# Kernel tuning notes

Hardware: AMD Instinct MI355X
Metric: run time of the kernel (lower is better)

## Reference

```python
import jax, jax.numpy as jnp
import numpy as np

T, K, D, CIN = 8, 64, 512, 1536  # timesteps, num_centers, redu_dim, input channels


def _conv(x, w, b=None, pad=0):
    y = jax.lax.conv_general_dilated(x, w, (1, 1), [(pad, pad), (pad, pad)],
                                     dimension_numbers=('NCHW', 'OIHW', 'NCHW'))
    return y if b is None else y + b[None, :, None, None]


def setup_inputs() -> dict:
    key = jax.random.key(0)
    ks = jax.random.split(key, 15)
    B, H, W = 32, 8, 8
    s = lambda i, shp: jax.random.normal(ks[i], shp, jnp.float32) * 0.05
    return dict(
        x=jax.random.normal(ks[0], (B * T, CIN, H, W), jnp.float32),
        redu_w=s(1, (D, CIN, 1, 1)), redu_b=s(2, (D,)),
        w_x=s(3, (K, D, 1, 1)),
        att_x=s(4, (K, K, 3, 3)), att_h_w=s(5, (K, K, 3, 3)), att_b=s(6, (K,)),
        share_w=s(7, (K, K, 3, 3)), share_b=s(8, (K,)),
        U_r=s(9, (K, K, 3, 3)), U_z=s(10, (K, K, 3, 3)), U_h=s(11, (K, K, 3, 3)),
        centers=s(12, (K, D)),
        fc1_w=s(13, (T * K // 16, T * K)), fc2_w=s(14, (T * K, T * K // 16)),
    )


def reference(x, redu_w, redu_b, w_x, att_x, att_h_w, att_b, share_w, share_b,
              U_r, U_z, U_h, centers, fc1_w, fc2_w):
    NT, _, H, W = x.shape
    B = NT // T
    xt = _conv(x, redu_w, redu_b)                    # (B*T, D, H, W) 1x1 reduction
    wxpb = _conv(xt, w_x)                            # (B*T, K, H, W)
    att_v = _conv(wxpb, att_x, pad=1).reshape(B, T, K, H, W).transpose(1, 0, 2, 3, 4)  # (T,B,K,H,W)
    wxpb5 = wxpb.reshape(B, T, K, H, W)

    def fc(v):  # ChannelAttention shared MLP (1x1 convs == matmuls)
        return jnp.maximum(v @ fc1_w.T, 0.) @ fc2_w.T

    def step(h, _):
        ah = _conv(h, att_h_w, att_b, pad=1)               # (B,K,H,W)
        e = jax.nn.relu(att_v + ah[None])                  # (T,B,K,H,W)
        e = e.transpose(1, 0, 2, 3, 4).reshape(B, T * K, H * W)
        g = jnp.tanh(fc(e.mean(-1)) + fc(e.max(-1)))       # (B, T*K) channel attention
        ex = jnp.exp(g.reshape(B, T, K))
        den = ex.sum(1, keepdims=True)
        den = den + (den == 0).astype(ex.dtype)
        alphas = ex / den                                  # softmax over timesteps
        wxt = (alphas[:, :, :, None, None] * wxpb5).sum(1) # (B,K,H,W)
        wxt = _conv(wxt, share_w, share_b, pad=1)
        z = jax.nn.sigmoid(wxt + _conv(h, U_z, pad=1))
        r = jax.nn.sigmoid(wxt + _conv(h, U_r, pad=1))
        hh = jnp.tanh(wxt + _conv(r * h, U_h, pad=1))
        h_new = (1. - z) * hh + z * h
        return h_new, h_new

    h0 = jnp.zeros((B, K, H, W), x.dtype)
    _, hs = jax.lax.scan(step, h0, None, length=T)         # (T,B,K,H,W)
    assigns = hs.transpose(1, 0, 2, 3, 4).reshape(B * T, K, H * W)
    a_sum = assigns.sum(-1, keepdims=True)                 # (B*T,K,1)
    a = a_sum * centers[None]                              # (B*T,K,D)
    feats = xt.reshape(B * T, D, H * W).transpose(0, 2, 1) # (B*T,HW,D)
    vlad = jnp.einsum('nks,nsd->nkd', assigns, feats) - a  # (B*T,K,D)
    vlad = vlad.reshape(B, T, K, D).sum(1)                 # (B,K,D)
    vlad = vlad / jnp.maximum(jnp.linalg.norm(vlad, axis=2, keepdims=True), 1e-12)
    vlad = vlad.reshape(B, K * D)
    vlad = vlad / jnp.maximum(jnp.linalg.norm(vlad, axis=1, keepdims=True), 1e-12)
    return vlad
```

## Files before the change

kernel.cpp:

```cpp
#include <hip/hip_runtime.h>
#include <math.h>

#define T_   8
#define K_   64
#define D_   512
#define CIN_ 1536
#define B_   32
#define S_   64
#define NT_  256

#define WLO_BF16  786432u
#define WXT_OFF   786432u
#define XT_OFF    819200u
#define WXPB_OFF  9207808u
#define ATTV_OFF  10256384u
#define HS_OFF    11436032u
#define ASUM_OFF  13041664u
#define WPB       25034752u

typedef __bf16 v8bf __attribute__((ext_vector_type(8)));
typedef __bf16 v4bf __attribute__((ext_vector_type(4)));
typedef float  v4f  __attribute__((ext_vector_type(4)));
typedef _Float16 v4h __attribute__((ext_vector_type(4)));
typedef _Float16 v8h __attribute__((ext_vector_type(8)));

__global__ __launch_bounds__(256) void k_prep(const float* __restrict__ redu_w,
                                              const float* __restrict__ w_x,
                                              float* __restrict__ ws) {
    unsigned idx = blockIdx.x * 256u + threadIdx.x;
    if (idx < 786432u) {
        float f = redu_w[idx];
        __bf16 h = (__bf16)f;
        __bf16 l = (__bf16)(f - (float)h);
        __bf16* wb = (__bf16*)ws;
        wb[idx] = h;
        wb[WLO_BF16 + idx] = l;
    } else if (idx < 819200u) {
        unsigned i = idx - 786432u;
        unsigned dd = i >> 6, k = i & 63u;
        ws[WXT_OFF + i] = w_x[k * 512u + dd];
    }
}

__global__ __launch_bounds__(256) void k_prep_w(const float* __restrict__ w0,
                                                const float* __restrict__ w1,
                                                const float* __restrict__ w2,
                                                const float* __restrict__ w3,
                                                const float* __restrict__ w4,
                                                float* __restrict__ ws) {
    unsigned idx = blockIdx.x * 256u + threadIdx.x;
    if (idx >= 184320u) return;
    unsigned w = idx / 36864u, r = idx % 36864u;
    const float* src = (w == 0) ? w0 : (w == 1) ? w1 : (w == 2) ? w2 : (w == 3) ? w3 : w4;
    float f = src[r];
    __bf16 h = (__bf16)f;
    __bf16 l = (__bf16)(f - (float)h);
    unsigned o = r / 576u, rem = r % 576u, ii = rem / 9u, dydx = rem % 9u;
    __bf16* wb = (__bf16*)ws;
    unsigned dst = WPB + w * 73728u + (dydx * 64u + o) * 64u + ii;
    wb[dst] = h;
    wb[dst + 36864u] = l;
}

__global__ __launch_bounds__(256) void k_gemm_xt_mfma(const float* __restrict__ x,
                                                      const float* __restrict__ redu_b,
                                                      float* __restrict__ ws) {
    __shared__ __bf16 xhi_s[64 * 72];
    __shared__ __bf16 xlo_s[64 * 72];
    const __bf16* __restrict__ Whi = (const __bf16*)ws;
    const __bf16* __restrict__ Wlo = ((const __bf16*)ws) + WLO_BF16;
    float* xt = ws + XT_OFF;
    const int n = blockIdx.y;
    const int d0 = blockIdx.x * 256;
    const int tid = threadIdx.x;
    const int wave = tid >> 6, lane = tid & 63;
    const int lrow = lane & 15, lkg = lane >> 4;
    const int m_base = d0 + wave * 64;
    const float* __restrict__ xn = x + n * 98304;
    const int s4 = tid & 15, cb = tid >> 4;

    v4f acc[4][4];
#pragma unroll
    for (int mt = 0; mt < 4; ++mt)
#pragma unroll
        for (int nt = 0; nt < 4; ++nt) acc[mt][nt] = (v4f){0.f, 0.f, 0.f, 0.f};

    for (int c0 = 0; c0 < 1536; c0 += 64) {
        float4 v[4];
#pragma unroll
        for (int j = 0; j < 4; ++j)
            v[j] = *(const float4*)&xn[(c0 + cb * 4 + j) * 64 + s4 * 4];
        __syncthreads();
#pragma unroll
        for (int i = 0; i < 4; ++i) {
            v4bf hv, lv;
#pragma unroll
            for (int j = 0; j < 4; ++j) {
                float f = ((const float*)&v[j])[i];
                __bf16 h = (__bf16)f;
                hv[j] = h;
                lv[j] = (__bf16)(f - (float)h);
            }
            int row = s4 * 4 + i;
            *(v4bf*)&xhi_s[row * 72 + cb * 4] = hv;
            *(v4bf*)&xlo_s[row * 72 + cb * 4] = lv;
        }
        __syncthreads();
#pragma unroll
        for (int ks = 0; ks < 64; ks += 32) {
            v8bf bh[4], bl[4], ah[4], al[4];
#pragma unroll
            for (int nt = 0; nt < 4; ++nt) {
                int off = (nt * 16 + lrow) * 72 + ks + lkg * 8;
                bh[nt] = *(const v8bf*)&xhi_s[off];
                bl[nt] = *(const v8bf*)&xlo_s[off];
            }
#pragma unroll
            for (int mt = 0; mt < 4; ++mt) {
                int gi = (m_base + mt * 16 + lrow) * 1536 + c0 + ks + lkg * 8;
                ah[mt] = *(const v8bf*)&Whi[gi];
                al[mt] = *(const v8bf*)&Wlo[gi];
            }
#pragma unroll
            for (int mt = 0; mt < 4; ++mt)
#pragma unroll
                for (int nt = 0; nt < 4; ++nt) {
                    acc[mt][nt] = __builtin_amdgcn_mfma_f32_16x16x32_bf16(
                        ah[mt], bh[nt], acc[mt][nt], 0, 0, 0);
                    acc[mt][nt] = __builtin_amdgcn_mfma_f32_16x16x32_bf16(
                        ah[mt], bl[nt], acc[mt][nt], 0, 0, 0);
                    acc[mt][nt] = __builtin_amdgcn_mfma_f32_16x16x32_bf16(
                        al[mt], bh[nt], acc[mt][nt], 0, 0, 0);
                }
        }
    }
#pragma unroll
    for (int mt = 0; mt < 4; ++mt) {
#pragma unroll
        for (int r = 0; r < 4; ++r) {
            int m = m_base + mt * 16 + lkg * 4 + r;
            float bias = redu_b[m];
#pragma unroll
            for (int nt = 0; nt < 4; ++nt) {
                int s = nt * 16 + lrow;
                xt[(n * 512 + m) * 64 + s] = acc[mt][nt][r] + bias;
            }
        }
    }
}

__global__ __launch_bounds__(256) void k_gemm_wxpb(float* __restrict__ ws) {
    __shared__ float Aw[16 * 64];
    __shared__ float Bx[16 * 64];
    const float* wxT = ws + WXT_OFF;
    const float* xt = ws + XT_OFF;
    float* wxpb = ws + WXPB_OFF;
    const int n = blockIdx.x;
    const int tid = threadIdx.x;
    const int sg = tid & 15, kg = tid >> 4;

    float acc[4][4];
#pragma unroll
    for (int i = 0; i < 4; ++i)
#pragma unroll
        for (int j = 0; j < 4; ++j) acc[i][j] = 0.f;

    for (int d0 = 0; d0 < 512; d0 += 16) {
        int cc = tid >> 4, q = tid & 15;
        *(float4*)&Aw[cc * 64 + q * 4] = *(const float4*)&wxT[(d0 + cc) * 64 + q * 4];
        *(float4*)&Bx[cc * 64 + q * 4] = *(const float4*)&xt[n * 32768 + (d0 + cc) * 64 + q * 4];
        __syncthreads();
#pragma unroll
        for (int c2 = 0; c2 < 16; ++c2) {
            float4 a = *(const float4*)&Aw[c2 * 64 + kg * 4];
            float4 b = *(const float4*)&Bx[c2 * 64 + sg * 4];
            float av[4] = {a.x, a.y, a.z, a.w};
            float bv[4] = {b.x, b.y, b.z, b.w};
#pragma unroll
            for (int i = 0; i < 4; ++i)
#pragma unroll
                for (int j = 0; j < 4; ++j)
                    acc[i][j] = fmaf(av[i], bv[j], acc[i][j]);
        }
        __syncthreads();
    }
#pragma unroll
    for (int i = 0; i < 4; ++i) {
        float4 o = {acc[i][0], acc[i][1], acc[i][2], acc[i][3]};
        *(float4*)&wxpb[(n * 64 + kg * 4 + i) * 64 + sg * 4] = o;
    }
}

__global__ __launch_bounds__(128) void k_conv3x3(const float* __restrict__ in,
                                                 const float* __restrict__ wt,
                                                 const float* __restrict__ bias,
                                                 float* __restrict__ out) {
    __shared__ float in_s[4096];
    __shared__ float w_s[16 * 576];
    const int img = blockIdx.y;
    const int k0 = blockIdx.x * 16;
    const int tid = threadIdx.x;
    const int kl = tid >> 3, y = tid & 7;
#pragma unroll
    for (int i = 0; i < 8; ++i) {
        int f = tid + i * 128;
        *(float4*)&in_s[f * 4] = *(const float4*)&in[img * 4096 + f * 4];
    }
#pragma unroll
    for (int i = 0; i < 18; ++i) {
        int f = tid + i * 128;
        *(float4*)&w_s[f * 4] = *(const float4*)&wt[k0 * 576 + f * 4];
    }
    __syncthreads();
    float o[8];
#pragma unroll
    for (int xx = 0; xx < 8; ++xx) o[xx] = 0.f;
    for (int kp = 0; kp < 64; ++kp) {
        const float* wp = &w_s[kl * 576 + kp * 9];
        float wv[9];
#pragma unroll
        for (int q = 0; q < 9; ++q) wv[q] = wp[q];
#pragma unroll
        for (int dy = 0; dy < 3; ++dy) {
            int yy = y + dy - 1;
            if (yy >= 0 && yy < 8) {
                float4 ra = *(const float4*)&in_s[kp * 64 + yy * 8];
                float4 rb = *(const float4*)&in_s[kp * 64 + yy * 8 + 4];
                float r[8] = {ra.x, ra.y, ra.z, ra.w, rb.x, rb.y, rb.z, rb.w};
                float wa = wv[dy * 3 + 0], wb = wv[dy * 3 + 1], wc = wv[dy * 3 + 2];
#pragma unroll
                for (int xx = 0; xx < 8; ++xx) {
                    float t = wb * r[xx];
                    if (xx > 0) t += wa * r[xx - 1];
                    if (xx < 7) t += wc * r[xx + 1];
                    o[xx] += t;
                }
            }
        }
    }
    float bv = bias ? bias[k0 + kl] : 0.f;
    float4 o0 = {o[0] + bv, o[1] + bv, o[2] + bv, o[3] + bv};
    float4 o1 = {o[4] + bv, o[5] + bv, o[6] + bv, o[7] + bv};
    *(float4*)&out[img * 4096 + (k0 + kl) * 64 + y * 8] = o0;
    *(float4*)&out[img * 4096 + (k0 + kl) * 64 + y * 8 + 4] = o1;
}

__device__ __forceinline__ void conv_mfma(const __bf16* __restrict__ Wh,
                                          const __bf16* tS,
                                          int l15, int kg8, int mt, v4f acc[4]) {
    v8bf vz;
#pragma unroll
    for (int q = 0; q < 8; ++q) vz[q] = (__bf16)0.f;
#pragma unroll
    for (int i = 0; i < 4; ++i) acc[i] = (v4f){0.f, 0.f, 0.f, 0.f};
    const int yb = l15 >> 3, xb = l15 & 7;
    v8bf wh[9][2];
#pragma unroll
    for (int p = 0; p < 9; ++p) {
        const int wrow = (p * 64 + mt * 16 + l15) * 64 + kg8;
#pragma unroll
        for (int kci = 0; kci < 2; ++kci)
            wh[p][kci] = *(const v8bf*)&Wh[wrow + kci * 32];
    }
#pragma unroll
    for (int dy = 0; dy < 3; ++dy)
#pragma unroll
        for (int dx = 0; dx < 3; ++dx) {
            const int x0 = xb + dx - 1;
            const bool okx = (unsigned)x0 < 8u;
#pragma unroll
            for (int i = 0; i < 4; ++i) {
                const int y0 = yb + dy - 1 + 2 * i;
                const bool ok = ((unsigned)y0 < 8u) & okx;
                const int s0 = ((y0 * 8 + x0) & 63) * 72 + kg8;
#pragma unroll
                for (int kci = 0; kci < 2; ++kci) {
                    v8bf b = ok ? *(const v8bf*)&tS[s0 + kci * 32] : vz;
                    acc[i] = __builtin_amdgcn_mfma_f32_16x16x32_bf16(
                        wh[dy * 3 + dx][kci], b, acc[i], 0, 0, 0);
                }
            }
        }
}

__device__ __forceinline__ void conv_mfma3(const __bf16* __restrict__ W0,
                                           const __bf16* __restrict__ W1,
                                           const __bf16* __restrict__ W2,
                                           const __bf16* tS,
                                           int l15, int kg8, int mt,
                                           v4f a0[4], v4f a1[4], v4f a2[4]) {
    v8bf vz;
#pragma unroll
    for (int q = 0; q < 8; ++q) vz[q] = (__bf16)0.f;
#pragma unroll
    for (int i = 0; i < 4; ++i) {
        a0[i] = (v4f){0.f, 0.f, 0.f, 0.f};
        a1[i] = (v4f){0.f, 0.f, 0.f, 0.f};
        a2[i] = (v4f){0.f, 0.f, 0.f, 0.f};
    }
    const int yb = l15 >> 3, xb = l15 & 7;
#pragma unroll
    for (int dy = 0; dy < 3; ++dy) {
        v8bf w0[3][2], w1[3][2], w2[3][2];
#pragma unroll
        for (int dx = 0; dx < 3; ++dx) {
            const int wrow = ((dy * 3 + dx) * 64 + mt * 16 + l15) * 64 + kg8;
#pragma unroll
            for (int kci = 0; kci < 2; ++kci) {
                w0[dx][kci] = *(const v8bf*)&W0[wrow + kci * 32];
                w1[dx][kci] = *(const v8bf*)&W1[wrow + kci * 32];
                w2[dx][kci] = *(const v8bf*)&W2[wrow + kci * 32];
            }
        }
#pragma unroll
        for (int dx = 0; dx < 3; ++dx) {
            const int x0 = xb + dx - 1;
            const bool okx = (unsigned)x0 < 8u;
#pragma unroll
            for (int i = 0; i < 4; ++i) {
                const int y0 = yb + dy - 1 + 2 * i;
                const bool ok = ((unsigned)y0 < 8u) & okx;
                const int s0 = ((y0 * 8 + x0) & 63) * 72 + kg8;
#pragma unroll
                for (int kci = 0; kci < 2; ++kci) {
                    v8bf b = ok ? *(const v8bf*)&tS[s0 + kci * 32] : vz;
                    a0[i] = __builtin_amdgcn_mfma_f32_16x16x32_bf16(w0[dx][kci], b, a0[i], 0, 0, 0);
                    a1[i] = __builtin_amdgcn_mfma_f32_16x16x32_bf16(w1[dx][kci], b, a1[i], 0, 0, 0);
                    a2[i] = __builtin_amdgcn_mfma_f32_16x16x32_bf16(w2[dx][kci], b, a2[i], 0, 0, 0);
                }
            }
        }
    }
}

__global__ __launch_bounds__(256) void k_recur(const float* __restrict__ att_b,
                                               const float* __restrict__ share_b,
                                               const float* __restrict__ fc1_w,
                                               const float* __restrict__ fc2_w,
                                               float* __restrict__ ws) {
    __shared__ float h_s[4096];
    __shared__ __attribute__((aligned(16))) __bf16 tA[64 * 72];
    __shared__ float cA[64 * 65];
    __shared__ float cB[64 * 65];
    __shared__ float misc[1088];
    __shared__ __attribute__((aligned(16))) _Float16 attv_s[32768];
    const int b = blockIdx.x, tid = threadIdx.x;
    const int lane = tid & 63;
    const int wave = tid >> 6;
    const int mt = wave;
    const int l15 = lane & 15, kg = lane >> 4, kg8 = kg * 8;
    const __bf16* Wp = (const __bf16*)ws + WPB;
    const float* attv = ws + ATTV_OFF;
    const float* wxpb = ws + WXPB_OFF;
    float* hsg = ws + HS_OFF;
    float* asg = ws + ASUM_OFF;

    {
        const float* src = attv + b * 32768;
        for (int i = tid; i < 8192; i += 256) {
            float4 v = *(const float4*)&src[i * 4];
            v4h h4 = {(_Float16)v.x, (_Float16)v.y, (_Float16)v.z, (_Float16)v.w};
            *(v4h*)&attv_s[i * 4] = h4;
        }
    }

    for (int i = tid; i < 4096; i += 256) h_s[i] = 0.f;
    float abvr[2];
#pragma unroll
    for (int rep = 0; rep < 2; ++rep) abvr[rep] = att_b[(tid + rep * 256) >> 3];
    float sb4[4];
#pragma unroll
    for (int r = 0; r < 4; ++r) sb4[r] = share_b[mt * 16 + kg * 4 + r];
    __syncthreads();

    for (int t = 0; t < 8; ++t) {
#pragma unroll
        for (int rep = 0; rep < 2; ++rep) {
            int s = tid & 63, g = (tid >> 6) + rep * 4;
#pragma unroll
            for (int q4 = 0; q4 < 2; ++q4) {
                v4bf hv;
#pragma unroll
                for (int q = 0; q < 4; ++q) hv[q] = (__bf16)h_s[(g * 8 + q4 * 4 + q) * 64 + s];
                *(v4bf*)&tA[s * 72 + g * 8 + q4 * 4] = hv;
            }
        }
        __syncthreads();
        v4f az[4], ar[4];
        {
            v4f a[4];
            conv_mfma3(Wp, Wp + 2u * 73728u, Wp + 3u * 73728u, tA,
                       l15, kg8, mt, a, az, ar);
#pragma unroll
            for (int i = 0; i < 4; ++i)
#pragma unroll
                for (int r = 0; r < 4; ++r)
                    cA[(mt * 16 + kg * 4 + r) * 65 + i * 16 + l15] = a[i][r];
        }
        __syncthreads();
#pragma unroll
        for (int rep = 0; rep < 2; ++rep) {
            int vt = tid + rep * 256;
            int kk = vt >> 3, yy = vt & 7;
            float ah8[8];
            const float* cr = &cA[kk * 65 + yy * 8];
#pragma unroll
            for (int xx = 0; xx < 8; ++xx) ah8[xx] = cr[xx] + abvr[rep];
            for (int tp = 0; tp < 8; ++tp) {
                v8h va = *(const v8h*)&attv_s[tp * 4096 + kk * 64 + yy * 8];
                float s_ = 0.f, m_ = 0.f;
#pragma unroll
                for (int xx = 0; xx < 8; ++xx) {
                    float v = fmaxf((float)va[xx] + ah8[xx], 0.f);
                    s_ += v;
                    m_ = fmaxf(m_, v);
                }
                s_ += __shfl_down(s_, 4, 8);
                s_ += __shfl_down(s_, 2, 8);
                s_ += __shfl_down(s_, 1, 8);
                m_ = fmaxf(m_, __shfl_down(m_, 4, 8));
                m_ = fmaxf(m_, __shfl_down(m_, 2, 8));
                m_ = fmaxf(m_, __shfl_down(m_, 1, 8));
                if (yy == 0) {
                    misc[tp * 64 + kk] = s_ * (1.f / 64.f);
                    misc[512 + tp * 64 + kk] = m_;
                }
            }
        }
        __syncthreads();
        {
            int i2 = tid >> 2, part = tid & 3;
            int i = i2 & 31;
            const float* src = misc + ((i2 < 32) ? 0 : 512);
            const float* wrow = fc1_w + i * 512 + part * 128;
            const float* s2 = src + part * 128;
            float p = 0.f;
#pragma unroll
            for (int c4 = 0; c4 < 32; ++c4) {
                float4 wv = *(const float4*)&wrow[c4 * 4];
                float4 sv = *(const float4*)&s2[c4 * 4];
                p = fmaf(wv.x, sv.x, p);
                p = fmaf(wv.y, sv.y, p);
                p = fmaf(wv.z, sv.z, p);
                p = fmaf(wv.w, sv.w, p);
            }
            p += __shfl_down(p, 2, 4);
            p += __shfl_down(p, 1, 4);
            if (part == 0) misc[1024 + i2] = fmaxf(p, 0.f);
        }
        __syncthreads();
#pragma unroll
        for (int rep = 0; rep < 2; ++rep) {
            int vt = tid + rep * 256;
            const float* w2 = fc2_w + vt * 32;
            float gm = 0.f, gx = 0.f;
#pragma unroll
            for (int i4 = 0; i4 < 8; ++i4) {
                float4 wv = *(const float4*)&w2[i4 * 4];
                gm = fmaf(wv.x, misc[1024 + i4 * 4 + 0], gm);
                gm = fmaf(wv.y, misc[1024 + i4 * 4 + 1], gm);
                gm = fmaf(wv.z, misc[1024 + i4 * 4 + 2], gm);
                gm = fmaf(wv.w, misc[1024 + i4 * 4 + 3], gm);
                gx = fmaf(wv.x, misc[1056 + i4 * 4 + 0], gx);
                gx = fmaf(wv.y, misc[1056 + i4 * 4 + 1], gx);
                gx = fmaf(wv.z, misc[1056 + i4 * 4 + 2], gx);
                gx = fmaf(wv.w, misc[1056 + i4 * 4 + 3], gx);
            }
            misc[vt] = expf(tanhf(gm + gx));
        }
        __syncthreads();
#pragma unroll
        for (int rep = 0; rep < 2; ++rep) {
            int vt = tid + rep * 256;
            int k6 = vt & 63;
            float den = 0.f;
#pragma unroll
            for (int tp = 0; tp < 8; ++tp) den += misc[tp * 64 + k6];
            den += (den == 0.f) ? 1.f : 0.f;
            misc[512 + vt] = misc[vt] / den;
        }
        __syncthreads();
#pragma unroll
        for (int rep = 0; rep < 2; ++rep) {
            int vt = tid + rep * 256;
            int kk = vt >> 3, yy = vt & 7;
            float wx8[8];
#pragma unroll
            for (int xx = 0; xx < 8; ++xx) wx8[xx] = 0.f;
            const float* src0 = wxpb + b * 32768 + kk * 64 + yy * 8;
#pragma unroll
            for (int tp = 0; tp < 8; ++tp) {
                float al = misc[512 + tp * 64 + kk];
                float4 v0 = *(const float4*)&src0[tp * 4096];
                float4 v1 = *(const float4*)&src0[tp * 4096 + 4];
                float v[8] = {v0.x, v0.y, v0.z, v0.w, v1.x, v1.y, v1.z, v1.w};
#pragma unroll
                for (int xx = 0; xx < 8; ++xx) wx8[xx] = fmaf(al, v[xx], wx8[xx]);
            }
#pragma unroll
            for (int xx = 0; xx < 8; ++xx) tA[(yy * 8 + xx) * 72 + kk] = (__bf16)wx8[xx];
        }
        __syncthreads();
        v4f ash[4];
        conv_mfma(Wp + 1u * 73728u, tA, l15, kg8, mt, ash);
        float zf[4][4], wof[4][4];
#pragma unroll
        for (int i = 0; i < 4; ++i)
#pragma unroll
            for (int r = 0; r < 4; ++r) {
                int ko = mt * 16 + kg * 4 + r;
                int s = i * 16 + l15;
                float wo = ash[i][r] + sb4[r];
                float z = 1.f / (1.f + expf(-(wo + az[i][r])));
                float rr = 1.f / (1.f + expf(-(wo + ar[i][r])));
                cB[ko * 65 + s] = rr * h_s[ko * 64 + s];
                zf[i][r] = z;
                wof[i][r] = wo;
            }
        __syncthreads();
#pragma unroll
        for (int rep = 0; rep < 2; ++rep) {
            int s = tid & 63, g = (tid >> 6) + rep * 4;
#pragma unroll
            for (int q4 = 0; q4 < 2; ++q4) {
                v4bf hv;
#pragma unroll
                for (int q = 0; q < 4; ++q) hv[q] = (__bf16)cB[(g * 8 + q4 * 4 + q) * 65 + s];
                *(v4bf*)&tA[s * 72 + g * 8 + q4 * 4] = hv;
            }
        }
        __syncthreads();
        {
            v4f ach[4];
            conv_mfma(Wp + 4u * 73728u, tA, l15, kg8, mt, ach);
#pragma unroll
            for (int r = 0; r < 4; ++r) {
                int ko = mt * 16 + kg * 4 + r;
                float rsum = 0.f;
#pragma unroll
                for (int i = 0; i < 4; ++i) {
                    int s = i * 16 + l15;
                    float hh = tanhf(wof[i][r] + ach[i][r]);
                    float hold = h_s[ko * 64 + s];
                    float hn = (1.f - zf[i][r]) * hh + zf[i][r] * hold;
                    h_s[ko * 64 + s] = hn;
                    hsg[((t * 32 + b) * 64 + ko) * 64 + s] = hn;
                    rsum += hn;
                }
                rsum += __shfl_xor(rsum, 8, 16);
                rsum += __shfl_xor(rsum, 4, 16);
                rsum += __shfl_xor(rsum, 2, 16);
                rsum += __shfl_xor(rsum, 1, 16);
                if (l15 == 0) misc[1024 + ko] = rsum;
            }
        }
        __syncthreads();
        if (tid < 64) asg[b * 512 + t * 64 + tid] = misc[1024 + tid];
        __syncthreads();
    }
}

__global__ __launch_bounds__(256) void k_vlad(const float* __restrict__ centers,
                                              const float* __restrict__ ws,
                                              float* __restrict__ out) {
    __shared__ float As[16 * 68];
    __shared__ float Bs[16 * 68];
    const int b = blockIdx.y;
    const int d0 = blockIdx.x * 64;
    const int tid = threadIdx.x;
    const int kq = tid & 15, dq = tid >> 4;
    const int lk = tid >> 2, q = tid & 3;
    const float* hs = ws + HS_OFF;
    const float* xt = ws + XT_OFF;
    float acc[4][4];
#pragma unroll
    for (int i = 0; i < 4; ++i)
#pragma unroll
        for (int j = 0; j < 4; ++j) acc[i][j] = 0.f;

    for (int rc = 0; rc < 512; rc += 16) {
        int t = rc >> 6, hw0 = rc & 63;
        float4 va = *(const float4*)&hs[((t * 32 + b) * 64 + lk) * 64 + hw0 + q * 4];
        float4 vb = *(const float4*)&xt[(b * 8 + t) * 32768 + (d0 + lk) * 64 + hw0 + q * 4];
        __syncthreads();
        As[(q * 4 + 0) * 68 + lk] = va.x;
        As[(q * 4 + 1) * 68 + lk] = va.y;
        As[(q * 4 + 2) * 68 + lk] = va.z;
        As[(q * 4 + 3) * 68 + lk] = va.w;
        Bs[(q * 4 + 0) * 68 + lk] = vb.x;
        Bs[(q * 4 + 1) * 68 + lk] = vb.y;
        Bs[(q * 4 + 2) * 68 + lk] = vb.z;
        Bs[(q * 4 + 3) * 68 + lk] = vb.w;
        __syncthreads();
#pragma unroll
        for (int cc = 0; cc < 16; ++cc) {
            float4 a = *(const float4*)&As[cc * 68 + kq * 4];
            float4 bb = *(const float4*)&Bs[cc * 68 + dq * 4];
            float av[4] = {a.x, a.y, a.z, a.w};
            float bv[4] = {bb.x, bb.y, bb.z, bb.w};
#pragma unroll
            for (int i = 0; i < 4; ++i)
#pragma unroll
                for (int j = 0; j < 4; ++j)
                    acc[i][j] = fmaf(av[i], bv[j], acc[i][j]);
        }
    }
    const float* asum = ws + ASUM_OFF;
#pragma unroll
    for (int i = 0; i < 4; ++i) {
        int k = kq * 4 + i;
        float at = 0.f;
#pragma unroll
        for (int tp = 0; tp < 8; ++tp) at += asum[b * 512 + tp * 64 + k];
        float4 cen = *(const float4*)&centers[k * 512 + d0 + dq * 4];
        float4 o = {acc[i][0] - at * cen.x, acc[i][1] - at * cen.y,
                    acc[i][2] - at * cen.z, acc[i][3] - at * cen.w};
        *(float4*)&out[b * 32768 + k * 512 + d0 + dq * 4] = o;
    }
}

__global__ __launch_bounds__(64) void k_norm1(float* __restrict__ out) {
    const int b = blockIdx.x >> 6, k = blockIdx.x & 63;
    float* p = out + b * 32768 + k * 512;
    const int tid = threadIdx.x;
    float v[8];
    float ss = 0.f;
#pragma unroll
    for (int i = 0; i < 8; ++i) {
        v[i] = p[tid + i * 64];
        ss = fmaf(v[i], v[i], ss);
    }
#pragma unroll
    for (int off = 32; off > 0; off >>= 1) ss += __shfl_down(ss, off, 64);
    ss = __shfl(ss, 0, 64);
    float sc = 1.f / fmaxf(sqrtf(ss), 1e-12f);
#pragma unroll
    for (int i = 0; i < 8; ++i) p[tid + i * 64] = v[i] * sc;
}

__global__ __launch_bounds__(256) void k_norm2(float* __restrict__ out) {
    __shared__ float red[4];
    __shared__ float stot;
    const int b = blockIdx.x;
    const int tid = threadIdx.x;
    float* p = out + b * 32768;
    float ss = 0.f;
    for (int i = 0; i < 32; ++i) {
        float4 v = *(const float4*)&p[tid * 4 + i * 1024];
        ss += v.x * v.x + v.y * v.y + v.z * v.z + v.w * v.w;
    }
#pragma unroll
    for (int off = 32; off > 0; off >>= 1) ss += __shfl_down(ss, off, 64);
    if ((tid & 63) == 0) red[tid >> 6] = ss;
    __syncthreads();
    if (tid == 0) stot = 1.f / fmaxf(sqrtf(red[0] + red[1] + red[2] + red[3]), 1e-12f);
    __syncthreads();
    float sc = stot;
    for (int i = 0; i < 32; ++i) {
        float4 v = *(const float4*)&p[tid * 4 + i * 1024];
        v.x *= sc; v.y *= sc; v.z *= sc; v.w *= sc;
        *(float4*)&p[tid * 4 + i * 1024] = v;
    }
}

extern "C" void kernel_launch(void* const* d_in, const int* in_sizes, int n_in,
                              void* d_out, int out_size, void* d_ws, size_t ws_size,
                              hipStream_t stream) {
    const float* x       = (const float*)d_in[0];
    const float* redu_w  = (const float*)d_in[1];
    const float* redu_b  = (const float*)d_in[2];
    const float* w_x     = (const float*)d_in[3];
    const float* att_x   = (const float*)d_in[4];
    const float* att_h_w = (const float*)d_in[5];
    const float* att_b   = (const float*)d_in[6];
    const float* share_w = (const float*)d_in[7];
    const float* share_b = (const float*)d_in[8];
    const float* U_r     = (const float*)d_in[9];
    const float* U_z     = (const float*)d_in[10];
    const float* U_h     = (const float*)d_in[11];
    const float* centers = (const float*)d_in[12];
    const float* fc1_w   = (const float*)d_in[13];
    const float* fc2_w   = (const float*)d_in[14];
    float* ws = (float*)d_ws;
    float* out = (float*)d_out;

    k_prep<<<dim3(3200), dim3(256), 0, stream>>>(redu_w, w_x, ws);
    k_prep_w<<<dim3(720), dim3(256), 0, stream>>>(att_h_w, share_w, U_z, U_r, U_h, ws);
    k_gemm_xt_mfma<<<dim3(2, 256), dim3(256), 0, stream>>>(x, redu_b, ws);
    k_gemm_wxpb<<<dim3(256), dim3(256), 0, stream>>>(ws);
    k_conv3x3<<<dim3(4, 256), dim3(128), 0, stream>>>(ws + WXPB_OFF, att_x,
                                                      (const float*)nullptr, ws + ATTV_OFF);
    k_recur<<<dim3(32), dim3(256), 0, stream>>>(att_b, share_b, fc1_w, fc2_w, ws);
    k_vlad<<<dim3(8, 32), dim3(256), 0, stream>>>(centers, ws, out);
    k_norm1<<<dim3(2048), dim3(64), 0, stream>>>(out);
    k_norm2<<<dim3(32), dim3(256), 0, stream>>>(out);
}
```

Baseline: 737.7 us.

## Fuse att_x 3x3 conv into recurrence kernel using bf16 MFMA

Removes the standalone FP32 k_conv3x3 launch that computed att_v for all timesteps and wrote it to global memory. k_recur now computes att_v per batch inside the kernel with the bf16 MFMA conv helper, using att_x weights pre-packed by k_prep_w, and stores the result straight into shared memory as fp16. This saves a kernel launch and a global write plus read of att_v. The cost is extra serial work in k_recur, which runs on only 32 blocks, and lower precision because only the high bf16 part of the weights is used. The fc1 dot product also switches to four independent accumulators to shorten the dependency chain.

```diff
diff --git a/kernel.cpp b/kernel.cpp
--- a/kernel.cpp
+++ b/kernel.cpp
@@ -17,6 +17,7 @@
 #define HS_OFF    11436032u
 #define ASUM_OFF  13041664u
 #define WPB       25034752u
+#define WATTX_BF16 20512768u
 
 typedef __bf16 v8bf __attribute__((ext_vector_type(8)));
 typedef __bf16 v4bf __attribute__((ext_vector_type(4)));
@@ -47,19 +48,25 @@
                                                 const float* __restrict__ w2,
                                                 const float* __restrict__ w3,
                                                 const float* __restrict__ w4,
+                                                const float* __restrict__ w5,
                                                 float* __restrict__ ws) {
     unsigned idx = blockIdx.x * 256u + threadIdx.x;
-    if (idx >= 184320u) return;
+    if (idx >= 221184u) return;
     unsigned w = idx / 36864u, r = idx % 36864u;
-    const float* src = (w == 0) ? w0 : (w == 1) ? w1 : (w == 2) ? w2 : (w == 3) ? w3 : w4;
+    const float* src = (w == 0) ? w0 : (w == 1) ? w1 : (w == 2) ? w2
+                     : (w == 3) ? w3 : (w == 4) ? w4 : w5;
     float f = src[r];
     __bf16 h = (__bf16)f;
     __bf16 l = (__bf16)(f - (float)h);
     unsigned o = r / 576u, rem = r % 576u, ii = rem / 9u, dydx = rem % 9u;
     __bf16* wb = (__bf16*)ws;
-    unsigned dst = WPB + w * 73728u + (dydx * 64u + o) * 64u + ii;
-    wb[dst] = h;
-    wb[dst + 36864u] = l;
+    if (w < 5u) {
+        unsigned dst = WPB + w * 73728u + (dydx * 64u + o) * 64u + ii;
+        wb[dst] = h;
+        wb[dst + 36864u] = l;
+    } else {
+        wb[WATTX_BF16 + (dydx * 64u + o) * 64u + ii] = h;
+    }
 }
 
 __global__ __launch_bounds__(256) void k_gemm_xt_mfma(const float* __restrict__ x,
@@ -189,60 +196,6 @@
         float4 o = {acc[i][0], acc[i][1], acc[i][2], acc[i][3]};
         *(float4*)&wxpb[(n * 64 + kg * 4 + i) * 64 + sg * 4] = o;
     }
-}
-
-__global__ __launch_bounds__(128) void k_conv3x3(const float* __restrict__ in,
-                                                 const float* __restrict__ wt,
-                                                 const float* __restrict__ bias,
-                                                 float* __restrict__ out) {
-    __shared__ float in_s[4096];
-    __shared__ float w_s[16 * 576];
-    const int img = blockIdx.y;
-    const int k0 = blockIdx.x * 16;
-    const int tid = threadIdx.x;
-    const int kl = tid >> 3, y = tid & 7;
-#pragma unroll
-    for (int i = 0; i < 8; ++i) {
-        int f = tid + i * 128;
-        *(float4*)&in_s[f * 4] = *(const float4*)&in[img * 4096 + f * 4];
-    }
-#pragma unroll
-    for (int i = 0; i < 18; ++i) {
-        int f = tid + i * 128;
-        *(float4*)&w_s[f * 4] = *(const float4*)&wt[k0 * 576 + f * 4];
-    }
-    __syncthreads();
-    float o[8];
-#pragma unroll
-    for (int xx = 0; xx < 8; ++xx) o[xx] = 0.f;
-    for (int kp = 0; kp < 64; ++kp) {
-        const float* wp = &w_s[kl * 576 + kp * 9];
-        float wv[9];
-#pragma unroll
-        for (int q = 0; q < 9; ++q) wv[q] = wp[q];
-#pragma unroll
-        for (int dy = 0; dy < 3; ++dy) {
-            int yy = y + dy - 1;
-            if (yy >= 0 && yy < 8) {
-                float4 ra = *(const float4*)&in_s[kp * 64 + yy * 8];
-                float4 rb = *(const float4*)&in_s[kp * 64 + yy * 8 + 4];
-                float r[8] = {ra.x, ra.y, ra.z, ra.w, rb.x, rb.y, rb.z, rb.w};
-                float wa = wv[dy * 3 + 0], wb = wv[dy * 3 + 1], wc = wv[dy * 3 + 2];
-#pragma unroll
-                for (int xx = 0; xx < 8; ++xx) {
-                    float t = wb * r[xx];
-                    if (xx > 0) t += wa * r[xx - 1];
-                    if (xx < 7) t += wc * r[xx + 1];
-                    o[xx] += t;
-                }
-            }
-        }
-    }
-    float bv = bias ? bias[k0 + kl] : 0.f;
-    float4 o0 = {o[0] + bv, o[1] + bv, o[2] + bv, o[3] + bv};
-    float4 o1 = {o[4] + bv, o[5] + bv, o[6] + bv, o[7] + bv};
-    *(float4*)&out[img * 4096 + (k0 + kl) * 64 + y * 8] = o0;
-    *(float4*)&out[img * 4096 + (k0 + kl) * 64 + y * 8 + 4] = o1;
 }
 
 __device__ __forceinline__ void conv_mfma(const __bf16* __restrict__ Wh,
@@ -350,28 +303,37 @@
     const int mt = wave;
     const int l15 = lane & 15, kg = lane >> 4, kg8 = kg * 8;
     const __bf16* Wp = (const __bf16*)ws + WPB;
-    const float* attv = ws + ATTV_OFF;
+    const __bf16* Wattx = (const __bf16*)ws + WATTX_BF16;
     const float* wxpb = ws + WXPB_OFF;
     float* hsg = ws + HS_OFF;
     float* asg = ws + ASUM_OFF;
 
-    {
-        const float* src = attv + b * 32768;
-        for (int i = tid; i < 8192; i += 256) {
-            float4 v = *(const float4*)&src[i * 4];
-            v4h h4 = {(_Float16)v.x, (_Float16)v.y, (_Float16)v.z, (_Float16)v.w};
-            *(v4h*)&attv_s[i * 4] = h4;
-        }
-    }
-
     for (int i = tid; i < 4096; i += 256) h_s[i] = 0.f;
+
+    for (int tp = 0; tp < 8; ++tp) {
+        const float* src = wxpb + (b * 8 + tp) * 4096;
+        for (int i = tid; i < 4096; i += 256) {
+            int k = i >> 6, s = i & 63;
+            tA[s * 72 + k] = (__bf16)src[i];
+        }
+        __syncthreads();
+        v4f av[4];
+        conv_mfma(Wattx, tA, l15, kg8, mt, av);
+#pragma unroll
+        for (int i2 = 0; i2 < 4; ++i2)
+#pragma unroll
+            for (int r = 0; r < 4; ++r)
+                attv_s[tp * 4096 + (mt * 16 + kg * 4 + r) * 64 + i2 * 16 + l15] =
+                    (_Float16)av[i2][r];
+        __syncthreads();
+    }
+
     float abvr[2];
 #pragma unroll
     for (int rep = 0; rep < 2; ++rep) abvr[rep] = att_b[(tid + rep * 256) >> 3];
     float sb4[4];
 #pragma unroll
     for (int r = 0; r < 4; ++r) sb4[r] = share_b[mt * 16 + kg * 4 + r];
-    __syncthreads();
 
     for (int t = 0; t < 8; ++t) {
 #pragma unroll
@@ -434,16 +396,18 @@
             const float* src = misc + ((i2 < 32) ? 0 : 512);
             const float* wrow = fc1_w + i * 512 + part * 128;
             const float* s2 = src + part * 128;
-            float p = 0.f;
+            float pa[4] = {0.f, 0.f, 0.f, 0.f};
 #pragma unroll
             for (int c4 = 0; c4 < 32; ++c4) {
                 float4 wv = *(const float4*)&wrow[c4 * 4];
                 float4 sv = *(const float4*)&s2[c4 * 4];
-                p = fmaf(wv.x, sv.x, p);
-                p = fmaf(wv.y, sv.y, p);
-                p = fmaf(wv.z, sv.z, p);
-                p = fmaf(wv.w, sv.w, p);
-            }
+                float* pp = &pa[c4 & 3];
+                *pp = fmaf(wv.x, sv.x, *pp);
+                *pp = fmaf(wv.y, sv.y, *pp);
+                *pp = fmaf(wv.z, sv.z, *pp);
+                *pp = fmaf(wv.w, sv.w, *pp);
+            }
+            float p = (pa[0] + pa[1]) + (pa[2] + pa[3]);
             p += __shfl_down(p, 2, 4);
             p += __shfl_down(p, 1, 4);
             if (part == 0) misc[1024 + i2] = fmaxf(p, 0.f);
@@ -685,11 +649,10 @@
     float* out = (float*)d_out;
 
     k_prep<<<dim3(3200), dim3(256), 0, stream>>>(redu_w, w_x, ws);
-    k_prep_w<<<dim3(720), dim3(256), 0, stream>>>(att_h_w, share_w, U_z, U_r, U_h, ws);
+    k_prep_w<<<dim3(864), dim3(256), 0, stream>>>(att_h_w, share_w, U_z, U_r, U_h,
+                                                  att_x, ws);
     k_gemm_xt_mfma<<<dim3(2, 256), dim3(256), 0, stream>>>(x, redu_b, ws);
     k_gemm_wxpb<<<dim3(256), dim3(256), 0, stream>>>(ws);
-    k_conv3x3<<<dim3(4, 256), dim3(128), 0, stream>>>(ws + WXPB_OFF, att_x,
-                                                      (const float*)nullptr, ws + ATTV_OFF);
     k_recur<<<dim3(32), dim3(256), 0, stream>>>(att_b, share_b, fc1_w, fc2_w, ws);
     k_vlad<<<dim3(8, 32), dim3(256), 0, stream>>>(centers, ws, out);
     k_norm1<<<dim3(2048), dim3(64), 0, stream>>>(out);
```

New measurement: 697.8 us. 1.06x faster.
